# Kernel optimization log

Hardware: AMD Instinct MI355X
Metric: run time of the kernel (lower is better)

The kernel has to match this reference:

```python
import jax, jax.numpy as jnp
import numpy as np
from jax import lax

NCP = 9  # 3x3 control grid

def _control_points():
    s = int(np.sqrt(NCP))
    pts = np.zeros((NCP, 2), np.float32)
    for i in range(NCP):
        pts[i, 0] = (i % s) / (s - 1) * 2 - 1
        pts[i, 1] = (i // s) / (s - 1) * 2 - 1
    return jnp.asarray(pts)

def _tps_L():
    cp = _control_points()
    d = cp[:, None, :] - cp[None, :, :]
    r2 = (d ** 2).sum(-1)
    r2s = jnp.where(r2 > 0, r2, 1.0)
    K = jnp.where(r2 > 0, r2s * jnp.log(r2s), 0.0)          # [9,9]
    P = jnp.concatenate([jnp.ones((NCP, 1)), cp], axis=1)   # [9,3]
    top = jnp.concatenate([K, P], axis=1)                   # [9,12]
    bot = jnp.concatenate([P.T, jnp.zeros((3, 3))], axis=1) # [3,12]
    return jnp.concatenate([top, bot], axis=0)              # [12,12]

def _conv(x, w, b):
    y = lax.conv_general_dilated(x, w, (1, 1), 'SAME',
                                 dimension_numbers=('NCHW', 'OIHW', 'NCHW'))
    return y + b[None, :, None, None]

def _maxpool2(x):
    return lax.reduce_window(x, -jnp.inf, lax.max, (1, 1, 2, 2), (1, 1, 2, 2), 'VALID')

def _grid_sample(img, grid):
    # bilinear, align_corners=True, zeros padding. img [B,C,H,W], grid [B,H,W,2]
    B, C, H, W = img.shape
    x = (grid[..., 0] + 1.0) * 0.5 * (W - 1)
    y = (grid[..., 1] + 1.0) * 0.5 * (H - 1)
    x0 = jnp.floor(x); y0 = jnp.floor(y)
    wx = x - x0; wy = y - y0
    def gather(ix, iy):
        valid = (ix >= 0) & (ix < W) & (iy >= 0) & (iy < H)
        ixc = jnp.clip(ix, 0, W - 1).astype(jnp.int32)
        iyc = jnp.clip(iy, 0, H - 1).astype(jnp.int32)
        v = jax.vmap(lambda im, yy, xx: im[:, yy, xx])(img, iyc, ixc)  # [B,C,Hg,Wg]
        return v * valid[:, None, :, :].astype(img.dtype)
    v00 = gather(x0, y0); v10 = gather(x0 + 1, y0)
    v01 = gather(x0, y0 + 1); v11 = gather(x0 + 1, y0 + 1)
    w00 = ((1 - wx) * (1 - wy))[:, None]; w10 = (wx * (1 - wy))[:, None]
    w01 = ((1 - wx) * wy)[:, None];       w11 = (wx * wy)[:, None]
    return v00 * w00 + v10 * w10 + v01 * w01 + v11 * w11

def setup_inputs() -> dict:
    key = jax.random.key(0)
    ks = jax.random.split(key, 9)
    B, C, H, W = 32, 1, 256, 256
    x = jax.random.normal(ks[0], (B, C, H, W), jnp.float32)
    def he(k, shape, fan_in):
        return jax.random.normal(k, shape, jnp.float32) * np.sqrt(2.0 / fan_in)
    return {
        'x': x,
        'conv1_w': he(ks[1], (32, 1, 3, 3), 1 * 9),   'conv1_b': jnp.zeros((32,)),
        'conv2_w': he(ks[2], (64, 32, 3, 3), 32 * 9), 'conv2_b': jnp.zeros((64,)),
        'fc1_w': he(ks[3], (256, 1024), 1024),        'fc1_b': jnp.zeros((256,)),
        'fc2_w': he(ks[4], (18, 256), 256) * 0.01,    'fc2_b': jnp.zeros((18,)),
    }

def reference(x, conv1_w, conv1_b, conv2_w, conv2_b, fc1_w, fc1_b, fc2_w, fc2_b):
    B, C, H, W = x.shape
    cp = _control_points()
    L = _tps_L()
    # localization network
    f = jax.nn.relu(_maxpool2(_conv(x, conv1_w, conv1_b)))
    f = jax.nn.relu(_maxpool2(_conv(f, conv2_w, conv2_b)))
    # adaptive avg pool to 4x4 (divisible case)
    Bh, Ch, Hh, Wh = f.shape
    f = f.reshape(Bh, Ch, 4, Hh // 4, 4, Wh // 4).mean(axis=(3, 5))
    f = f.reshape(B, -1)
    h = jax.nn.relu(f @ fc1_w.T + fc1_b)
    disp = (h @ fc2_w.T + fc2_b).reshape(B, NCP, 2)
    target = cp[None] + disp                                  # [B,9,2]
    # batched 12x12 TPS solve
    Y = jnp.concatenate([target, jnp.zeros((B, 3, 2))], axis=1)  # [B,12,2]
    Wfull = jnp.linalg.solve(jnp.broadcast_to(L, (B, 12, 12)), Y)
    Wc, A = Wfull[:, :NCP], Wfull[:, NCP:]                    # [B,9,2], [B,3,2]
    # identity sampling grid (align_corners=True)
    xs = jnp.linspace(-1.0, 1.0, W)
    ys = jnp.linspace(-1.0, 1.0, H)
    gx, gy = jnp.meshgrid(xs, ys)                             # [H,W]
    pts = jnp.stack([gx, gy], axis=-1).reshape(1, H * W, 2)   # [1,N,2]
    # RBF warp
    diffs = pts[:, :, None, :] - cp[None, None, :, :]         # [1,N,9,2]
    r2 = (diffs ** 2).sum(-1)                                 # [1,N,9]
    r2s = jnp.where(r2 > 0, r2, 1.0)
    U = jnp.where(r2 > 0, r2s * jnp.log(r2s), 0.0)            # [1,N,9]
    warp = jnp.einsum('xnk,bkd->bnd', U, Wc)                  # [B,N,2]
    affine = A[:, 0:1] + A[:, 1:2] * pts[..., 0:1] + A[:, 2:3] * pts[..., 1:2]
    wgrid = (affine + warp).reshape(B, H, W, 2)
    return _grid_sample(x, wgrid)
```

## Files before the change

kernel.cpp:

```cpp
#include <hip/hip_runtime.h>
#include <hip/hip_bf16.h>
#include <math.h>

#define BATCH 32
#define IMG 256
#define NCP 9
#define F1P 130

typedef __attribute__((ext_vector_type(8))) short bf16x8;
typedef __attribute__((ext_vector_type(4))) float f32x4;
typedef __attribute__((ext_vector_type(4))) unsigned int uint4v;

__device__ __constant__ float d_cpx[9] = {-1.f,0.f,1.f,-1.f,0.f,1.f,-1.f,0.f,1.f};
__device__ __constant__ float d_cpy[9] = {-1.f,-1.f,-1.f,0.f,0.f,0.f,1.f,1.f,1.f};

__device__ inline unsigned int pack2bf(float a, float b) {
    __hip_bfloat16 ha = __float2bfloat16(a), hb = __float2bfloat16(b);
    unsigned short ua = *(unsigned short*)&ha, ub = *(unsigned short*)&hb;
    return ((unsigned int)ub << 16) | ua;
}

__global__ __launch_bounds__(256) void k_conv1p(const float* __restrict__ x,
        const float* __restrict__ w, const float* __restrict__ bias,
        __hip_bfloat16* __restrict__ f1, const float* __restrict__ w2c,
        __hip_bfloat16* __restrict__ wt, float* __restrict__ linv) {
    int blk = blockIdx.x;
    if (blk >= 2048) {
        int pblk = blk - 2048;
        if (pblk == 0) {
            int j = threadIdx.x;
            if (j >= 24) return;
            const float cx[9] = {-1,0,1,-1,0,1,-1,0,1};
            const float cy[9] = {-1,-1,-1,0,0,0,1,1,1};
            float col[12];
            #pragma unroll
            for (int i = 0; i < 12; ++i) {
                float v;
                if (j < 12) {
                    if (i < 9 && j < 9) {
                        float dx = cx[i] - cx[j], dy = cy[i] - cy[j];
                        float r2 = dx * dx + dy * dy;
                        v = (r2 > 0.f) ? r2 * logf(r2) : 0.f;
                    } else if (i < 9) {
                        v = (j == 9) ? 1.f : ((j == 10) ? cx[i] : cy[i]);
                    } else if (j < 9) {
                        v = (i == 9) ? 1.f : ((i == 10) ? cx[j] : cy[j]);
                    } else v = 0.f;
                } else v = (i == j - 12) ? 1.f : 0.f;
                col[i] = v;
            }
            #pragma unroll
            for (int c = 0; c < 12; ++c) {
                float f[12];
                #pragma unroll
                for (int i = 0; i < 12; ++i) f[i] = __shfl(col[i], c);
                int p = c; float best = fabsf(f[c]);
                #pragma unroll
                for (int r = 0; r < 12; ++r) if (r > c) {
                    float a = fabsf(f[r]);
                    bool g = a > best;
                    best = g ? a : best;
                    p = g ? r : p;
                }
                float oldc = col[c], colp = col[c];
                #pragma unroll
                for (int r = 0; r < 12; ++r) colp = (r == p) ? col[r] : colp;
                #pragma unroll
                for (int r = 0; r < 12; ++r) col[r] = (r == p) ? oldc : col[r];
                col[c] = colp;
                float oldfc = f[c], fpv = f[c];
                #pragma unroll
                for (int r = 0; r < 12; ++r) fpv = (r == p) ? f[r] : fpv;
                #pragma unroll
                for (int r = 0; r < 12; ++r) f[r] = (r == p) ? oldfc : f[r];
                f[c] = fpv;
                float inv = 1.0f / f[c];
                col[c] *= inv;
                #pragma unroll
                for (int r = 0; r < 12; ++r) if (r != c) col[r] = fmaf(-f[r], col[c], col[r]);
            }
            if (j >= 12) {
                #pragma unroll
                for (int i = 0; i < 12; ++i) linv[i * 12 + (j - 12)] = col[i];
            }
            return;
        }
        int t = (pblk - 1) * 256 + threadIdx.x;
        if (t < 18432) {
            int pos = t / 2048, rem = t % 2048, oc = rem >> 5, ic = rem & 31;
            wt[t] = __float2bfloat16(w2c[(oc * 32 + ic) * 9 + pos]);
            return;
        }
        int u = t - 18432;
        if (u < 32 * 2064) {
            int b = u / 2064, q = u % 2064;
            int row, px, ch;
            if (q < 520)       { row = 0;   px = q >> 2;         ch = q & 3; }
            else if (q < 1040) { row = 129; px = (q - 520) >> 2; ch = q & 3; }
            else { int z = q - 1040; row = 1 + (z >> 3); int tt = z & 7;
                   px = (tt < 4) ? 0 : 129; ch = tt & 3; }
            uint4v zero = {0, 0, 0, 0};
            size_t eo = ((((size_t)b * F1P + row) * F1P + px) * 32 + ch * 8);
            *(uint4v*)((char*)f1 + eo * 2) = zero;
        }
        return;
    }
    int tj = blk & 7, ti = (blk >> 3) & 7, b = blk >> 6;
    __shared__ float tile[34 * 34];
    __shared__ float wl[32 * 9];
    __shared__ float bl[32];
    int tid = threadIdx.x;
    for (int i = tid; i < 32 * 9; i += 256) wl[i] = w[i];
    if (tid < 32) bl[tid] = bias[tid];
    const float* xb = x + (size_t)b * IMG * IMG;
    int oy0 = ti * 32 - 1, ox0 = tj * 32 - 1;
    for (int i = tid; i < 34 * 34; i += 256) {
        int yy = i / 34, xx = i % 34;
        int r = oy0 + yy, c = ox0 + xx;
        float v = 0.f;
        if (r >= 0 && r < IMG && c >= 0 && c < IMG) v = xb[r * IMG + c];
        tile[i] = v;
    }
    __syncthreads();
    int oy = tid >> 4, ox = tid & 15;
    float p[16];
    #pragma unroll
    for (int yy = 0; yy < 4; ++yy)
        #pragma unroll
        for (int xx = 0; xx < 4; ++xx)
            p[yy * 4 + xx] = tile[(2 * oy + yy) * 34 + (2 * ox + xx)];
    int gy = ti * 16 + oy, gx = tj * 16 + ox;
    unsigned int u[16];
    #pragma unroll
    for (int oc2 = 0; oc2 < 16; ++oc2) {
        float vv[2];
        #pragma unroll
        for (int h = 0; h < 2; ++h) {
            int oc = oc2 * 2 + h;
            float ww[9];
            #pragma unroll
            for (int k = 0; k < 9; ++k) ww[k] = wl[oc * 9 + k];
            float m = -INFINITY;
            #pragma unroll
            for (int dy = 0; dy < 2; ++dy)
                #pragma unroll
                for (int dx = 0; dx < 2; ++dx) {
                    float s = 0.f;
                    #pragma unroll
                    for (int ky = 0; ky < 3; ++ky)
                        #pragma unroll
                        for (int kx = 0; kx < 3; ++kx)
                            s = fmaf(p[(dy + ky) * 4 + dx + kx], ww[ky * 3 + kx], s);
                    m = fmaxf(m, s);
                }
            vv[h] = fmaxf(m + bl[oc], 0.f);
        }
        u[oc2] = pack2bf(vv[0], vv[1]);
    }
    size_t eo = (((size_t)b * F1P + (gy + 1)) * F1P + (gx + 1)) * 32;
    uint4v* dst = (uint4v*)((char*)f1 + eo * 2);
    #pragma unroll
    for (int q = 0; q < 4; ++q) {
        uint4v vq = { u[q*4+0], u[q*4+1], u[q*4+2], u[q*4+3] };
        dst[q] = vq;
    }
}

__global__ __launch_bounds__(512) void k_conv2m(const __hip_bfloat16* __restrict__ f1,
        const __hip_bfloat16* __restrict__ wt, const float* __restrict__ bias,
        float* __restrict__ feat) {
    __shared__ float red[8][64];
    int tid = threadIdx.x;
    int w = tid >> 6, l = tid & 63;
    int lr = l & 15, lg = l >> 4;
    int blk = blockIdx.x;
    int region = blk & 15;
    int b = blk >> 4;
    int ry = region >> 2, rx = region & 3;
    const __hip_bfloat16* f1b = f1 + (size_t)b * F1P * F1P * 32;

    bf16x8 Bf[4][9];
    #pragma unroll
    for (int n = 0; n < 4; ++n)
        #pragma unroll
        for (int p = 0; p < 9; ++p)
            Bf[n][p] = *(const bf16x8*)(wt + ((size_t)(p * 64 + n * 16 + lr) * 32 + lg * 8));
    float biasv[4];
    #pragma unroll
    for (int n = 0; n < 4; ++n) biasv[n] = bias[n * 16 + lr];

    float fsum[4] = {0.f, 0.f, 0.f, 0.f};

    #pragma unroll 1
    for (int b4 = 0; b4 < 2; ++b4) {
        int pr = b4 * 8 + w;
        int row0 = ry * 32 + 2 * pr;
        #pragma unroll
        for (int xt = 0; xt < 2; ++xt) {
            int x0 = rx * 32 + xt * 16 + lr;
            bf16x8 Af[4][3];
            #pragma unroll
            for (int rr = 0; rr < 4; ++rr)
                #pragma unroll
                for (int dx = 0; dx < 3; ++dx)
                    Af[rr][dx] = *(const bf16x8*)(f1b + ((size_t)(row0 + rr) * F1P + x0 + dx) * 32 + lg * 8);
            #pragma unroll
            for (int n = 0; n < 4; ++n) {
                f32x4 a0 = {0.f, 0.f, 0.f, 0.f}, a1 = {0.f, 0.f, 0.f, 0.f};
                #pragma unroll
                for (int dy = 0; dy < 3; ++dy)
                    #pragma unroll
                    for (int dx = 0; dx < 3; ++dx) {
                        a0 = __builtin_amdgcn_mfma_f32_16x16x32_bf16(Af[dy][dx],     Bf[n][dy * 3 + dx], a0, 0, 0, 0);
                        a1 = __builtin_amdgcn_mfma_f32_16x16x32_bf16(Af[dy + 1][dx], Bf[n][dy * 3 + dx], a1, 0, 0, 0);
                    }
                float p0 = fmaxf(fmaxf(a0[0], a0[1]), fmaxf(a1[0], a1[1]));
                float p1 = fmaxf(fmaxf(a0[2], a0[3]), fmaxf(a1[2], a1[3]));
                fsum[n] += fmaxf(p0 + biasv[n], 0.f) + fmaxf(p1 + biasv[n], 0.f);
            }
        }
    }

    #pragma unroll
    for (int n = 0; n < 4; ++n) {
        fsum[n] += __shfl_xor(fsum[n], 16);
        fsum[n] += __shfl_xor(fsum[n], 32);
    }
    if (l < 16) {
        #pragma unroll
        for (int n = 0; n < 4; ++n) red[w][n * 16 + l] = fsum[n];
    }
    __syncthreads();
    if (tid < 64) {
        float s = 0.f;
        #pragma unroll
        for (int ww = 0; ww < 8; ++ww) s += red[ww][tid];
        feat[(size_t)b * 1024 + tid * 16 + region] = s * (1.0f / 256.0f);
    }
}

__global__ __launch_bounds__(256) void k_fc1(const float* __restrict__ feat,
        const float* __restrict__ w, const float* __restrict__ bias,
        float* __restrict__ h) {
    int wave = threadIdx.x >> 6, lane = threadIdx.x & 63;
    int o = blockIdx.x * 4 + wave;
    int j = o & 255, g = o >> 8;
    const float4* wr = (const float4*)(w + (size_t)j * 1024);
    const float4* fb0 = (const float4*)(feat + (size_t)(g * 4 + 0) * 1024);
    const float4* fb1 = (const float4*)(feat + (size_t)(g * 4 + 1) * 1024);
    const float4* fb2 = (const float4*)(feat + (size_t)(g * 4 + 2) * 1024);
    const float4* fb3 = (const float4*)(feat + (size_t)(g * 4 + 3) * 1024);
    float s0 = 0.f, s1 = 0.f, s2 = 0.f, s3 = 0.f;
    #pragma unroll
    for (int i = 0; i < 4; ++i) {
        float4 a = wr[lane + i * 64];
        float4 c0 = fb0[lane + i * 64];
        float4 c1 = fb1[lane + i * 64];
        float4 c2 = fb2[lane + i * 64];
        float4 c3 = fb3[lane + i * 64];
        s0 = fmaf(a.x, c0.x, s0); s0 = fmaf(a.y, c0.y, s0);
        s0 = fmaf(a.z, c0.z, s0); s0 = fmaf(a.w, c0.w, s0);
        s1 = fmaf(a.x, c1.x, s1); s1 = fmaf(a.y, c1.y, s1);
        s1 = fmaf(a.z, c1.z, s1); s1 = fmaf(a.w, c1.w, s1);
        s2 = fmaf(a.x, c2.x, s2); s2 = fmaf(a.y, c2.y, s2);
        s2 = fmaf(a.z, c2.z, s2); s2 = fmaf(a.w, c2.w, s2);
        s3 = fmaf(a.x, c3.x, s3); s3 = fmaf(a.y, c3.y, s3);
        s3 = fmaf(a.z, c3.z, s3); s3 = fmaf(a.w, c3.w, s3);
    }
    #pragma unroll
    for (int off = 32; off; off >>= 1) {
        s0 += __shfl_xor(s0, off);
        s1 += __shfl_xor(s1, off);
        s2 += __shfl_xor(s2, off);
        s3 += __shfl_xor(s3, off);
    }
    if (lane == 0) {
        float bj = bias[j];
        h[(size_t)(g * 4 + 0) * 256 + j] = fmaxf(s0 + bj, 0.f);
        h[(size_t)(g * 4 + 1) * 256 + j] = fmaxf(s1 + bj, 0.f);
        h[(size_t)(g * 4 + 2) * 256 + j] = fmaxf(s2 + bj, 0.f);
        h[(size_t)(g * 4 + 3) * 256 + j] = fmaxf(s3 + bj, 0.f);
    }
}

__global__ __launch_bounds__(64) void k_head(const float* __restrict__ h,
        const float* __restrict__ w2, const float* __restrict__ b2,
        const float* __restrict__ linv, float* __restrict__ wfull) {
    int b = blockIdx.x;
    int t = threadIdx.x;
    __shared__ float Y[12][2];
    __shared__ float L[144];
    const float* hb = h + (size_t)b * 256;
    for (int i = t; i < 144; i += 64) L[i] = linv[i];
    if (t < 18) {
        const float* wr = w2 + (size_t)t * 256;
        float s = 0.f;
        for (int k = 0; k < 256; ++k) s = fmaf(wr[k], hb[k], s);
        s += b2[t];
        int kk = t >> 1, d = t & 1;
        float cp = (d == 0) ? d_cpx[kk] : d_cpy[kk];
        Y[kk][d] = cp + s;
    }
    if (t >= 18 && t < 24) Y[9 + ((t - 18) >> 1)][(t - 18) & 1] = 0.f;
    __syncthreads();
    if (t < 24) {
        int i = t >> 1, d = t & 1;
        float s = 0.f;
        #pragma unroll
        for (int k = 0; k < 12; ++k) s = fmaf(L[i * 12 + k], Y[k][d], s);
        wfull[b * 24 + i * 2 + d] = s;
    }
}

__global__ __launch_bounds__(256) void k_sample(const float* __restrict__ x,
        const float* __restrict__ wfull, float* __restrict__ out) {
    int py = blockIdx.x & 255;
    int bg = blockIdx.x >> 8;
    int px = threadIdx.x;
    __shared__ float Wf[8][24];
    if (threadIdx.x < 192) {
        int bi = threadIdx.x / 24, q = threadIdx.x % 24;
        Wf[bi][q] = wfull[(bg * 8 + bi) * 24 + q];
    }
    __syncthreads();
    float gx = px * (2.0f / 255.0f) - 1.0f;
    float gy = py * (2.0f / 255.0f) - 1.0f;
    float U[9];
    #pragma unroll
    for (int k = 0; k < 9; ++k) {
        float dx = gx - d_cpx[k], dy = gy - d_cpy[k];
        float r2 = dx * dx + dy * dy;
        U[k] = (r2 > 0.f) ? r2 * logf(r2) : 0.f;
    }
    #pragma unroll
    for (int bi = 0; bi < 8; ++bi) {
        int b = bg * 8 + bi;
        float sx = Wf[bi][18] + Wf[bi][20] * gx + Wf[bi][22] * gy;
        float sy = Wf[bi][19] + Wf[bi][21] * gx + Wf[bi][23] * gy;
        #pragma unroll
        for (int k = 0; k < 9; ++k) {
            sx = fmaf(U[k], Wf[bi][k * 2 + 0], sx);
            sy = fmaf(U[k], Wf[bi][k * 2 + 1], sy);
        }
        float xp = (sx + 1.0f) * 0.5f * 255.0f;
        float yp = (sy + 1.0f) * 0.5f * 255.0f;
        float x0f = floorf(xp), y0f = floorf(yp);
        float wx = xp - x0f, wy = yp - y0f;
        int x0 = (int)x0f, y0 = (int)y0f;
        const float* xb = x + (size_t)b * IMG * IMG;
        float v00, v10, v01, v11;
        {
            int ix, iy; bool valid; int ixc, iyc;
            ix = x0;     iy = y0;
            valid = (ix >= 0) && (ix < IMG) && (iy >= 0) && (iy < IMG);
            ixc = min(max(ix, 0), IMG - 1); iyc = min(max(iy, 0), IMG - 1);
            v00 = valid ? xb[iyc * IMG + ixc] : 0.f;
            ix = x0 + 1; iy = y0;
            valid = (ix >= 0) && (ix < IMG) && (iy >= 0) && (iy < IMG);
            ixc = min(max(ix, 0), IMG - 1); iyc = min(max(iy, 0), IMG - 1);
            v10 = valid ? xb[iyc * IMG + ixc] : 0.f;
            ix = x0;     iy = y0 + 1;
            valid = (ix >= 0) && (ix < IMG) && (iy >= 0) && (iy < IMG);
            ixc = min(max(ix, 0), IMG - 1); iyc = min(max(iy, 0), IMG - 1);
            v01 = valid ? xb[iyc * IMG + ixc] : 0.f;
            ix = x0 + 1; iy = y0 + 1;
            valid = (ix >= 0) && (ix < IMG) && (iy >= 0) && (iy < IMG);
            ixc = min(max(ix, 0), IMG - 1); iyc = min(max(iy, 0), IMG - 1);
            v11 = valid ? xb[iyc * IMG + ixc] : 0.f;
        }
        float r = v00 * (1.f - wx) * (1.f - wy) + v10 * wx * (1.f - wy)
                + v01 * (1.f - wx) * wy        + v11 * wx * wy;
        out[(size_t)b * IMG * IMG + py * IMG + px] = r;
    }
}

extern "C" void kernel_launch(void* const* d_in, const int* in_sizes, int n_in,
                              void* d_out, int out_size, void* d_ws, size_t ws_size,
                              hipStream_t stream) {
    const float* x   = (const float*)d_in[0];
    const float* c1w = (const float*)d_in[1];
    const float* c1b = (const float*)d_in[2];
    const float* c2w = (const float*)d_in[3];
    const float* c2b = (const float*)d_in[4];
    const float* w1  = (const float*)d_in[5];
    const float* b1  = (const float*)d_in[6];
    const float* w2  = (const float*)d_in[7];
    const float* b2  = (const float*)d_in[8];
    float* out = (float*)d_out;

    __hip_bfloat16* f1 = (__hip_bfloat16*)d_ws;
    __hip_bfloat16* wt = f1 + (size_t)32 * F1P * F1P * 32;
    float* fbase = (float*)(wt + 18432);
    float* feat  = fbase;
    float* hbuf  = feat + 32768;
    float* wfull = hbuf + 8192;
    float* linv  = wfull + 768;

    k_conv1p<<<2048 + 331, 256, 0, stream>>>(x, c1w, c1b, f1, c2w, wt, linv);
    k_conv2m<<<BATCH * 16, 512, 0, stream>>>(f1, wt, c2b, feat);
    k_fc1   <<<512, 256, 0, stream>>>(feat, w1, b1, hbuf);
    k_head  <<<BATCH, 64, 0, stream>>>(hbuf, w2, b2, linv, wfull);
    k_sample<<<1024, 256, 0, stream>>>(x, wfull, out);
}
```

Baseline: 74.62 us.

## Fuse conv1+pool into conv2 via shared-memory tiles, use fp16 dot2 for conv1

```diff
diff --git a/kernel.cpp b/kernel.cpp
--- a/kernel.cpp
+++ b/kernel.cpp
@@ -5,11 +5,17 @@
 #define BATCH 32
 #define IMG 256
 #define NCP 9
-#define F1P 130
 
 typedef __attribute__((ext_vector_type(8))) short bf16x8;
 typedef __attribute__((ext_vector_type(4))) float f32x4;
 typedef __attribute__((ext_vector_type(4))) unsigned int uint4v;
+typedef __attribute__((ext_vector_type(2))) _Float16 half2v;
+
+#if defined(__has_builtin)
+#if __has_builtin(__builtin_amdgcn_fdot2)
+#define HAS_FDOT2 1
+#endif
+#endif
 
 __device__ __constant__ float d_cpx[9] = {-1.f,0.f,1.f,-1.f,0.f,1.f,-1.f,0.f,1.f};
 __device__ __constant__ float d_cpy[9] = {-1.f,-1.f,-1.f,0.f,0.f,0.f,1.f,1.f,1.f};
@@ -20,164 +26,143 @@
     return ((unsigned int)ub << 16) | ua;
 }
 
-__global__ __launch_bounds__(256) void k_conv1p(const float* __restrict__ x,
-        const float* __restrict__ w, const float* __restrict__ bias,
-        __hip_bfloat16* __restrict__ f1, const float* __restrict__ w2c,
-        __hip_bfloat16* __restrict__ wt, float* __restrict__ linv) {
-    int blk = blockIdx.x;
-    if (blk >= 2048) {
-        int pblk = blk - 2048;
-        if (pblk == 0) {
-            int j = threadIdx.x;
-            if (j >= 24) return;
-            const float cx[9] = {-1,0,1,-1,0,1,-1,0,1};
-            const float cy[9] = {-1,-1,-1,0,0,0,1,1,1};
-            float col[12];
-            #pragma unroll
-            for (int i = 0; i < 12; ++i) {
-                float v;
-                if (j < 12) {
-                    if (i < 9 && j < 9) {
-                        float dx = cx[i] - cx[j], dy = cy[i] - cy[j];
-                        float r2 = dx * dx + dy * dy;
-                        v = (r2 > 0.f) ? r2 * logf(r2) : 0.f;
-                    } else if (i < 9) {
-                        v = (j == 9) ? 1.f : ((j == 10) ? cx[i] : cy[i]);
-                    } else if (j < 9) {
-                        v = (i == 9) ? 1.f : ((i == 10) ? cx[j] : cy[j]);
-                    } else v = 0.f;
-                } else v = (i == j - 12) ? 1.f : 0.f;
-                col[i] = v;
-            }
-            #pragma unroll
-            for (int c = 0; c < 12; ++c) {
-                float f[12];
-                #pragma unroll
-                for (int i = 0; i < 12; ++i) f[i] = __shfl(col[i], c);
-                int p = c; float best = fabsf(f[c]);
-                #pragma unroll
-                for (int r = 0; r < 12; ++r) if (r > c) {
-                    float a = fabsf(f[r]);
-                    bool g = a > best;
-                    best = g ? a : best;
-                    p = g ? r : p;
-                }
-                float oldc = col[c], colp = col[c];
-                #pragma unroll
-                for (int r = 0; r < 12; ++r) colp = (r == p) ? col[r] : colp;
-                #pragma unroll
-                for (int r = 0; r < 12; ++r) col[r] = (r == p) ? oldc : col[r];
-                col[c] = colp;
-                float oldfc = f[c], fpv = f[c];
-                #pragma unroll
-                for (int r = 0; r < 12; ++r) fpv = (r == p) ? f[r] : fpv;
-                #pragma unroll
-                for (int r = 0; r < 12; ++r) f[r] = (r == p) ? oldfc : f[r];
-                f[c] = fpv;
-                float inv = 1.0f / f[c];
-                col[c] *= inv;
-                #pragma unroll
-                for (int r = 0; r < 12; ++r) if (r != c) col[r] = fmaf(-f[r], col[c], col[r]);
-            }
-            if (j >= 12) {
-                #pragma unroll
-                for (int i = 0; i < 12; ++i) linv[i * 12 + (j - 12)] = col[i];
-            }
-            return;
-        }
-        int t = (pblk - 1) * 256 + threadIdx.x;
-        if (t < 18432) {
-            int pos = t / 2048, rem = t % 2048, oc = rem >> 5, ic = rem & 31;
-            wt[t] = __float2bfloat16(w2c[(oc * 32 + ic) * 9 + pos]);
-            return;
-        }
-        int u = t - 18432;
-        if (u < 32 * 2064) {
-            int b = u / 2064, q = u % 2064;
-            int row, px, ch;
-            if (q < 520)       { row = 0;   px = q >> 2;         ch = q & 3; }
-            else if (q < 1040) { row = 129; px = (q - 520) >> 2; ch = q & 3; }
-            else { int z = q - 1040; row = 1 + (z >> 3); int tt = z & 7;
-                   px = (tt < 4) ? 0 : 129; ch = tt & 3; }
-            uint4v zero = {0, 0, 0, 0};
-            size_t eo = ((((size_t)b * F1P + row) * F1P + px) * 32 + ch * 8);
-            *(uint4v*)((char*)f1 + eo * 2) = zero;
-        }
-        return;
-    }
-    int tj = blk & 7, ti = (blk >> 3) & 7, b = blk >> 6;
-    __shared__ float tile[34 * 34];
-    __shared__ float wl[32 * 9];
+__global__ __launch_bounds__(256) void k_prep(const float* __restrict__ w2c,
+        __hip_bfloat16* __restrict__ wt) {
+    int t = blockIdx.x * 256 + threadIdx.x;
+    if (t >= 18432) return;
+    int pos = t / 2048, rem = t % 2048, oc = rem >> 5, ic = rem & 31;
+    wt[t] = __float2bfloat16(w2c[(oc * 32 + ic) * 9 + pos]);
+}
+
+__global__ __launch_bounds__(512) void k_fused(const float* __restrict__ x,
+        const float* __restrict__ c1w, const float* __restrict__ c1b,
+        const __hip_bfloat16* __restrict__ wt, const float* __restrict__ c2b,
+        float* __restrict__ feat) {
+    __shared__ float xs[70 * 72];
+#if HAS_FDOT2
+    __shared__ unsigned wh2[160];
+#else
+    __shared__ float wl[288];
+#endif
     __shared__ float bl[32];
-    int tid = threadIdx.x;
-    for (int i = tid; i < 32 * 9; i += 256) wl[i] = w[i];
-    if (tid < 32) bl[tid] = bias[tid];
-    const float* xb = x + (size_t)b * IMG * IMG;
-    int oy0 = ti * 32 - 1, ox0 = tj * 32 - 1;
-    for (int i = tid; i < 34 * 34; i += 256) {
-        int yy = i / 34, xx = i % 34;
-        int r = oy0 + yy, c = ox0 + xx;
-        float v = 0.f;
-        if (r >= 0 && r < IMG && c >= 0 && c < IMG) v = xb[r * IMG + c];
-        tile[i] = v;
-    }
-    __syncthreads();
-    int oy = tid >> 4, ox = tid & 15;
-    float p[16];
-    #pragma unroll
-    for (int yy = 0; yy < 4; ++yy)
-        #pragma unroll
-        for (int xx = 0; xx < 4; ++xx)
-            p[yy * 4 + xx] = tile[(2 * oy + yy) * 34 + (2 * ox + xx)];
-    int gy = ti * 16 + oy, gx = tj * 16 + ox;
-    unsigned int u[16];
-    #pragma unroll
-    for (int oc2 = 0; oc2 < 16; ++oc2) {
-        float vv[2];
-        #pragma unroll
-        for (int h = 0; h < 2; ++h) {
-            int oc = oc2 * 2 + h;
-            float ww[9];
-            #pragma unroll
-            for (int k = 0; k < 9; ++k) ww[k] = wl[oc * 9 + k];
-            float m = -INFINITY;
-            #pragma unroll
-            for (int dy = 0; dy < 2; ++dy)
-                #pragma unroll
-                for (int dx = 0; dx < 2; ++dx) {
-                    float s = 0.f;
-                    #pragma unroll
-                    for (int ky = 0; ky < 3; ++ky)
-                        #pragma unroll
-                        for (int kx = 0; kx < 3; ++kx)
-                            s = fmaf(p[(dy + ky) * 4 + dx + kx], ww[ky * 3 + kx], s);
-                    m = fmaxf(m, s);
-                }
-            vv[h] = fmaxf(m + bl[oc], 0.f);
-        }
-        u[oc2] = pack2bf(vv[0], vv[1]);
-    }
-    size_t eo = (((size_t)b * F1P + (gy + 1)) * F1P + (gx + 1)) * 32;
-    uint4v* dst = (uint4v*)((char*)f1 + eo * 2);
-    #pragma unroll
-    for (int q = 0; q < 4; ++q) {
-        uint4v vq = { u[q*4+0], u[q*4+1], u[q*4+2], u[q*4+3] };
-        dst[q] = vq;
-    }
-}
-
-__global__ __launch_bounds__(512) void k_conv2m(const __hip_bfloat16* __restrict__ f1,
-        const __hip_bfloat16* __restrict__ wt, const float* __restrict__ bias,
-        float* __restrict__ feat) {
+    __shared__ bf16x8 f1v[4 * 34 * 34];
     __shared__ float red[8][64];
+
     int tid = threadIdx.x;
     int w = tid >> 6, l = tid & 63;
     int lr = l & 15, lg = l >> 4;
     int blk = blockIdx.x;
-    int region = blk & 15;
-    int b = blk >> 4;
+    int region = blk & 15, b = blk >> 4;
     int ry = region >> 2, rx = region & 3;
-    const __hip_bfloat16* f1b = f1 + (size_t)b * F1P * F1P * 32;
+
+    const float* xb = x + (size_t)b * IMG * IMG;
+    int xr0 = 64 * ry - 3, xc0 = 64 * rx - 3;
+    for (int i = tid; i < 70 * 70; i += 512) {
+        int r = i / 70, c = i - r * 70;
+        int gr = xr0 + r, gc = xc0 + c;
+        float v = 0.f;
+        if (gr >= 0 && gr < IMG && gc >= 0 && gc < IMG) v = xb[gr * IMG + gc];
+        xs[r * 72 + c] = v;
+    }
+#if HAS_FDOT2
+    if (tid < 160) {
+        int oc = tid / 5, q = tid - oc * 5;
+        float v0 = c1w[oc * 9 + 2 * q];
+        float v1 = (q < 4) ? c1w[oc * 9 + 2 * q + 1] : 0.f;
+        half2v hh; hh[0] = (_Float16)v0; hh[1] = (_Float16)v1;
+        wh2[tid] = *(unsigned*)&hh;
+    }
+#else
+    if (tid < 288) wl[tid] = c1w[tid];
+#endif
+    if (tid >= 192 && tid < 224) bl[tid - 192] = c1b[tid - 192];
+    __syncthreads();
+
+    #pragma unroll 1
+    for (int it = 0; it < 3; ++it) {
+        int px = tid + it * 512;
+        if (px >= 34 * 34) continue;
+        int fr = px / 34, fx = px - fr * 34;
+        int gfr = ry * 32 - 1 + fr, gfx = rx * 32 - 1 + fx;
+        unsigned u[16];
+        if (gfr >= 0 && gfr < 128 && gfx >= 0 && gfx < 128) {
+            float p[16];
+            #pragma unroll
+            for (int a = 0; a < 4; ++a)
+                #pragma unroll
+                for (int c = 0; c < 4; ++c)
+                    p[a * 4 + c] = xs[(2 * fr + a) * 72 + 2 * fx + c];
+#if HAS_FDOT2
+            half2v ap[4][5];
+            #pragma unroll
+            for (int pos = 0; pos < 4; ++pos) {
+                int dy = pos >> 1, dx = pos & 1;
+                float t9[9];
+                #pragma unroll
+                for (int ky = 0; ky < 3; ++ky)
+                    #pragma unroll
+                    for (int kx = 0; kx < 3; ++kx)
+                        t9[ky * 3 + kx] = p[(dy + ky) * 4 + dx + kx];
+                #pragma unroll
+                for (int q = 0; q < 4; ++q) {
+                    half2v hh; hh[0] = (_Float16)t9[2 * q]; hh[1] = (_Float16)t9[2 * q + 1];
+                    ap[pos][q] = hh;
+                }
+                half2v h8; h8[0] = (_Float16)t9[8]; h8[1] = (_Float16)0.f;
+                ap[pos][4] = h8;
+            }
+            float vprev = 0.f;
+            #pragma unroll
+            for (int oc = 0; oc < 32; ++oc) {
+                half2v wv[5];
+                #pragma unroll
+                for (int q = 0; q < 5; ++q) { unsigned uw = wh2[oc * 5 + q]; wv[q] = *(half2v*)&uw; }
+                float m = -INFINITY;
+                #pragma unroll
+                for (int pos = 0; pos < 4; ++pos) {
+                    float s = 0.f;
+                    #pragma unroll
+                    for (int q = 0; q < 5; ++q) s = __builtin_amdgcn_fdot2(ap[pos][q], wv[q], s, false);
+                    m = fmaxf(m, s);
+                }
+                float v = fmaxf(m + bl[oc], 0.f);
+                if (oc & 1) u[oc >> 1] = pack2bf(vprev, v); else vprev = v;
+            }
+#else
+            float vprev = 0.f;
+            #pragma unroll
+            for (int oc = 0; oc < 32; ++oc) {
+                float ww[9];
+                #pragma unroll
+                for (int k = 0; k < 9; ++k) ww[k] = wl[oc * 9 + k];
+                float m = -INFINITY;
+                #pragma unroll
+                for (int dy = 0; dy < 2; ++dy)
+                    #pragma unroll
+                    for (int dx = 0; dx < 2; ++dx) {
+                        float s = 0.f;
+                        #pragma unroll
+                        for (int ky = 0; ky < 3; ++ky)
+                            #pragma unroll
+                            for (int kx = 0; kx < 3; ++kx)
+                                s = fmaf(p[(dy + ky) * 4 + dx + kx], ww[ky * 3 + kx], s);
+                        m = fmaxf(m, s);
+                    }
+                float v = fmaxf(m + bl[oc], 0.f);
+                if (oc & 1) u[oc >> 1] = pack2bf(vprev, v); else vprev = v;
+            }
+#endif
+        } else {
+            #pragma unroll
+            for (int i = 0; i < 16; ++i) u[i] = 0u;
+        }
+        #pragma unroll
+        for (int g = 0; g < 4; ++g) {
+            uint4v vq = { u[g * 4 + 0], u[g * 4 + 1], u[g * 4 + 2], u[g * 4 + 3] };
+            f1v[g * 1156 + px] = *(bf16x8*)&vq;
+        }
+    }
+    __syncthreads();
 
     bf16x8 Bf[4][9];
     #pragma unroll
@@ -187,23 +172,20 @@
             Bf[n][p] = *(const bf16x8*)(wt + ((size_t)(p * 64 + n * 16 + lr) * 32 + lg * 8));
     float biasv[4];
     #pragma unroll
-    for (int n = 0; n < 4; ++n) biasv[n] = bias[n * 16 + lr];
+    for (int n = 0; n < 4; ++n) biasv[n] = c2b[n * 16 + lr];
 
     float fsum[4] = {0.f, 0.f, 0.f, 0.f};
-
     #pragma unroll 1
     for (int b4 = 0; b4 < 2; ++b4) {
         int pr = b4 * 8 + w;
-        int row0 = ry * 32 + 2 * pr;
         #pragma unroll
         for (int xt = 0; xt < 2; ++xt) {
-            int x0 = rx * 32 + xt * 16 + lr;
             bf16x8 Af[4][3];
             #pragma unroll
             for (int rr = 0; rr < 4; ++rr)
                 #pragma unroll
                 for (int dx = 0; dx < 3; ++dx)
-                    Af[rr][dx] = *(const bf16x8*)(f1b + ((size_t)(row0 + rr) * F1P + x0 + dx) * 32 + lg * 8);
+                    Af[rr][dx] = f1v[lg * 1156 + (2 * pr + rr) * 34 + xt * 16 + lr + dx];
             #pragma unroll
             for (int n = 0; n < 4; ++n) {
                 f32x4 a0 = {0.f, 0.f, 0.f, 0.f}, a1 = {0.f, 0.f, 0.f, 0.f};
@@ -234,7 +216,7 @@
     if (tid < 64) {
         float s = 0.f;
         #pragma unroll
-        for (int ww = 0; ww < 8; ++ww) s += red[ww][tid];
+        for (int ww2 = 0; ww2 < 8; ++ww2) s += red[ww2][tid];
         feat[(size_t)b * 1024 + tid * 16 + region] = s * (1.0f / 256.0f);
     }
 }
@@ -285,13 +267,67 @@
 
 __global__ __launch_bounds__(64) void k_head(const float* __restrict__ h,
         const float* __restrict__ w2, const float* __restrict__ b2,
-        const float* __restrict__ linv, float* __restrict__ wfull) {
+        float* __restrict__ wfull) {
     int b = blockIdx.x;
     int t = threadIdx.x;
-    __shared__ float Y[12][2];
     __shared__ float L[144];
+    __shared__ float Y[24];
+    if (t < 24) {
+        const float cx[9] = {-1,0,1,-1,0,1,-1,0,1};
+        const float cy[9] = {-1,-1,-1,0,0,0,1,1,1};
+        float col[12];
+        #pragma unroll
+        for (int i = 0; i < 12; ++i) {
+            float v;
+            if (t < 12) {
+                if (i < 9 && t < 9) {
+                    float dx = cx[i] - cx[t], dy = cy[i] - cy[t];
+                    float r2 = dx * dx + dy * dy;
+                    v = (r2 > 0.f) ? r2 * logf(r2) : 0.f;
+                } else if (i < 9) {
+                    v = (t == 9) ? 1.f : ((t == 10) ? cx[i] : cy[i]);
+                } else if (t < 9) {
+                    v = (i == 9) ? 1.f : ((i == 10) ? cx[t] : cy[t]);
+                } else v = 0.f;
+            } else v = (i == t - 12) ? 1.f : 0.f;
+            col[i] = v;
+        }
+        #pragma unroll
+        for (int c = 0; c < 12; ++c) {
+            float f[12];
+            #pragma unroll
+            for (int i = 0; i < 12; ++i) f[i] = __shfl(col[i], c);
+            int p = c; float best = fabsf(f[c]);
+            #pragma unroll
+            for (int r = 0; r < 12; ++r) if (r > c) {
+                float a = fabsf(f[r]);
+                bool g = a > best;
+                best = g ? a : best;
+                p = g ? r : p;
+            }
+            float oldc = col[c], colp = col[c];
+            #pragma unroll
+            for (int r = 0; r < 12; ++r) colp = (r == p) ? col[r] : colp;
+            #pragma unroll
+            for (int r = 0; r < 12; ++r) col[r] = (r == p) ? oldc : col[r];
+            col[c] = colp;
+            float oldfc = f[c], fpv = f[c];
+            #pragma unroll
+            for (int r = 0; r < 12; ++r) fpv = (r == p) ? f[r] : fpv;
+            #pragma unroll
+            for (int r = 0; r < 12; ++r) f[r] = (r == p) ? oldfc : f[r];
+            f[c] = fpv;
+            float inv = 1.0f / f[c];
+            col[c] *= inv;
+            #pragma unroll
+            for (int r = 0; r < 12; ++r) if (r != c) col[r] = fmaf(-f[r], col[c], col[r]);
+        }
+        if (t >= 12) {
+            #pragma unroll
+            for (int i = 0; i < 12; ++i) L[i * 12 + (t - 12)] = col[i];
+        }
+    }
     const float* hb = h + (size_t)b * 256;
-    for (int i = t; i < 144; i += 64) L[i] = linv[i];
     if (t < 18) {
         const float* wr = w2 + (size_t)t * 256;
         float s = 0.f;
@@ -299,16 +335,16 @@
         s += b2[t];
         int kk = t >> 1, d = t & 1;
         float cp = (d == 0) ? d_cpx[kk] : d_cpy[kk];
-        Y[kk][d] = cp + s;
-    }
-    if (t >= 18 && t < 24) Y[9 + ((t - 18) >> 1)][(t - 18) & 1] = 0.f;
+        Y[t] = cp + s;
+    }
+    if (t >= 18 && t < 24) Y[t] = 0.f;
     __syncthreads();
     if (t < 24) {
         int i = t >> 1, d = t & 1;
         float s = 0.f;
         #pragma unroll
-        for (int k = 0; k < 12; ++k) s = fmaf(L[i * 12 + k], Y[k][d], s);
-        wfull[b * 24 + i * 2 + d] = s;
+        for (int k = 0; k < 12; ++k) s = fmaf(L[i * 12 + k], Y[k * 2 + d], s);
+        wfull[b * 24 + t] = s;
     }
 }
 
@@ -388,17 +424,14 @@
     const float* b2  = (const float*)d_in[8];
     float* out = (float*)d_out;
 
-    __hip_bfloat16* f1 = (__hip_bfloat16*)d_ws;
-    __hip_bfloat16* wt = f1 + (size_t)32 * F1P * F1P * 32;
-    float* fbase = (float*)(wt + 18432);
-    float* feat  = fbase;
+    __hip_bfloat16* wt = (__hip_bfloat16*)d_ws;
+    float* feat  = (float*)((char*)d_ws + 36864);
     float* hbuf  = feat + 32768;
     float* wfull = hbuf + 8192;
-    float* linv  = wfull + 768;
-
-    k_conv1p<<<2048 + 331, 256, 0, stream>>>(x, c1w, c1b, f1, c2w, wt, linv);
-    k_conv2m<<<BATCH * 16, 512, 0, stream>>>(f1, wt, c2b, feat);
+
+    k_prep  <<<72, 256, 0, stream>>>(c2w, wt);
+    k_fused <<<BATCH * 16, 512, 0, stream>>>(x, c1w, c1b, wt, c2b, feat);
     k_fc1   <<<512, 256, 0, stream>>>(feat, w1, b1, hbuf);
-    k_head  <<<BATCH, 64, 0, stream>>>(hbuf, w2, b2, linv, wfull);
+    k_head  <<<BATCH, 64, 0, stream>>>(hbuf, w2, b2, wfull);
     k_sample<<<1024, 256, 0, stream>>>(x, wfull, out);
 }
```

New measurement: 76.83 us. +3.0%, slower.
